# Optimization experiments

Hardware: AMD Instinct MI355X
Metric: run time of the kernel (lower is better)

## Reference

```python
import jax, jax.numpy as jnp
import numpy as np

EMBEDDING_DIM = 64  # matches init_kwargs; temperature = sqrt(embedding_dim)


def setup_inputs() -> dict:
    key = jax.random.key(0)
    k1, k2, k3, k4 = jax.random.split(key, 4)
    B, S, D = 8, 2048, EMBEDDING_DIM
    return {
        "key": jax.random.normal(k1, (B, S, D), dtype=jnp.float32),
        "query": jax.random.normal(k2, (B, S, D), dtype=jnp.float32),
        "value": jax.random.normal(k3, (B, S, D), dtype=jnp.float32),
        "query_attention_mask": jax.random.randint(k4, (B, S), 0, 2, dtype=jnp.int32),
    }


def reference(key, query, value, query_attention_mask):
    # scores: [B, S, S]
    temperature = jnp.sqrt(jnp.asarray(EMBEDDING_DIM, dtype=query.dtype))
    scores = jnp.einsum("bqd,bkd->bqk", query, key) / temperature
    # masked_fill_ fills -inf WHERE mask is True (as in the torch source).
    # mask [B, S] -> broadcast over the query axis to [B, 1, S] -> [B, S, S].
    mask = query_attention_mask.astype(bool)[:, None, :]
    scores = jnp.where(mask, -jnp.inf, scores)
    attention_filter = jax.nn.softmax(scores, axis=-1)
    # dropout p=0.0 (deterministic reference) -> identity
    context = jnp.einsum("bqk,bkd->bqd", attention_filter, value)
    return (context, attention_filter)
```

## Files before the change

kernel.cpp:

```cpp
#include <hip/hip_runtime.h>
#include <hip/hip_bf16.h>
#include <math.h>


typedef short bf16x8 __attribute__((ext_vector_type(8)));
typedef short bf16x4 __attribute__((ext_vector_type(4)));
typedef float f32x4 __attribute__((ext_vector_type(4)));

#define BATCH 8
#define SDIM 2048
#define DDIM 64
#define KBLK 64
#define NBLK (SDIM / KBLK)
#define SCALE 0.125f

__device__ __forceinline__ short f2bf(float f) {
    unsigned x = __float_as_uint(f);
    x = (x + 0x7fffu + ((x >> 16) & 1u)) >> 16;
    return (short)x;
}

__device__ __forceinline__ float fidx(const float4& v, int i) {
    return ((const float*)&v)[i];
}

__global__ __launch_bounds__(256, 1)
void attn_fused(const float* __restrict__ Kg, const float* __restrict__ Qg,
                const float* __restrict__ Vg, const int* __restrict__ Mg,
                float* __restrict__ Ctx, float* __restrict__ Filt)
{
    __shared__ short Klds[KBLK][72];
    __shared__ short VTlds[DDIM][72];
    __shared__ float Plds[4][16][68];
    __shared__ int   Mlds[KBLK];

    const int wg = blockIdx.x;
    const int b = wg & 7;
    const int qtile = wg >> 3;
    const int tid = threadIdx.x;
    const int w = tid >> 6;
    const int lane = tid & 63;
    const int col = lane & 15;
    const int quad = lane >> 4;

    const float* Kb = Kg + (size_t)b * SDIM * DDIM;
    const float* Qb = Qg + (size_t)b * SDIM * DDIM;
    const float* Vb = Vg + (size_t)b * SDIM * DDIM;
    const int*   Mb = Mg + (size_t)b * SDIM;
    float* Ctxb  = Ctx  + (size_t)b * SDIM * DDIM;
    float* Filtb = Filt + (size_t)b * SDIM * SDIM;

    const int qrow = qtile * 64 + w * 16 + col;

    bf16x8 aq[2];
    {
        const float* qsrc = Qb + (size_t)qrow * DDIM + quad * 8;
        #pragma unroll
        for (int c = 0; c < 2; ++c) {
            float4 f0 = *(const float4*)(qsrc + c * 32);
            float4 f1 = *(const float4*)(qsrc + c * 32 + 4);
            bf16x8 a;
            a[0]=f2bf(f0.x); a[1]=f2bf(f0.y); a[2]=f2bf(f0.z); a[3]=f2bf(f0.w);
            a[4]=f2bf(f1.x); a[5]=f2bf(f1.y); a[6]=f2bf(f1.z); a[7]=f2bf(f1.w);
            aq[c] = a;
        }
    }

    const int sk_key = tid >> 2;
    const int sk_d0  = (tid & 3) * 16;
    const int sv_d0  = (tid & 15) * 4;
    const int sv_k0  = (tid >> 4) * 4;

    float m_run[4], l_run[4];
    #pragma unroll
    for (int r = 0; r < 4; ++r) { m_run[r] = -1e30f; l_run[r] = 0.0f; }

    float4 kreg[4];
    int mreg = 0;
    {
        const float* src = Kb + (size_t)sk_key * DDIM + sk_d0;
        #pragma unroll
        for (int i = 0; i < 4; ++i) kreg[i] = *(const float4*)(src + i * 4);
        if (tid < KBLK) mreg = Mb[tid];
    }

    for (int kb = 0; kb < NBLK; ++kb) {
        __syncthreads();
        {
            bf16x8 p0, p1;
            p0[0]=f2bf(kreg[0].x); p0[1]=f2bf(kreg[0].y); p0[2]=f2bf(kreg[0].z); p0[3]=f2bf(kreg[0].w);
            p0[4]=f2bf(kreg[1].x); p0[5]=f2bf(kreg[1].y); p0[6]=f2bf(kreg[1].z); p0[7]=f2bf(kreg[1].w);
            p1[0]=f2bf(kreg[2].x); p1[1]=f2bf(kreg[2].y); p1[2]=f2bf(kreg[2].z); p1[3]=f2bf(kreg[2].w);
            p1[4]=f2bf(kreg[3].x); p1[5]=f2bf(kreg[3].y); p1[6]=f2bf(kreg[3].z); p1[7]=f2bf(kreg[3].w);
            *(bf16x8*)&Klds[sk_key][sk_d0]     = p0;
            *(bf16x8*)&Klds[sk_key][sk_d0 + 8] = p1;
            if (tid < KBLK) Mlds[tid] = mreg;
        }
        __syncthreads();
        if (kb + 1 < NBLK) {
            const float* src = Kb + (size_t)((kb + 1) * KBLK + sk_key) * DDIM + sk_d0;
            #pragma unroll
            for (int i = 0; i < 4; ++i) kreg[i] = *(const float4*)(src + i * 4);
            if (tid < KBLK) mreg = Mb[(kb + 1) * KBLK + tid];
        }

        float s[4][4];
        #pragma unroll
        for (int t = 0; t < 4; ++t) {
            f32x4 acc = {0.f, 0.f, 0.f, 0.f};
            #pragma unroll
            for (int c = 0; c < 2; ++c) {
                bf16x8 bk = *(const bf16x8*)&Klds[t * 16 + col][c * 32 + quad * 8];
                acc = __builtin_amdgcn_mfma_f32_16x16x32_bf16(aq[c], bk, acc, 0, 0, 0);
            }
            const int mk = Mlds[t * 16 + col];
            #pragma unroll
            for (int r = 0; r < 4; ++r)
                s[t][r] = mk ? -INFINITY : acc[r] * SCALE;
        }
        #pragma unroll
        for (int r = 0; r < 4; ++r) {
            float mx = fmaxf(fmaxf(s[0][r], s[1][r]), fmaxf(s[2][r], s[3][r]));
            mx = fmaxf(mx, __shfl_xor(mx, 1));
            mx = fmaxf(mx, __shfl_xor(mx, 2));
            mx = fmaxf(mx, __shfl_xor(mx, 4));
            mx = fmaxf(mx, __shfl_xor(mx, 8));
            const float mn = fmaxf(m_run[r], mx);
            float sum = __expf(s[0][r] - mn) + __expf(s[1][r] - mn)
                      + __expf(s[2][r] - mn) + __expf(s[3][r] - mn);
            sum += __shfl_xor(sum, 1);
            sum += __shfl_xor(sum, 2);
            sum += __shfl_xor(sum, 4);
            sum += __shfl_xor(sum, 8);
            l_run[r] = l_run[r] * __expf(m_run[r] - mn) + sum;
            m_run[r] = mn;
        }
    }

    float inv_l[4];
    #pragma unroll
    for (int r = 0; r < 4; ++r) inv_l[r] = 1.0f / l_run[r];

    f32x4 Oacc[4];
    #pragma unroll
    for (int dt = 0; dt < 4; ++dt) Oacc[dt] = (f32x4){0.f, 0.f, 0.f, 0.f};

    float4 vreg[4];
    {
        const float* srck = Kb + (size_t)sk_key * DDIM + sk_d0;
        #pragma unroll
        for (int i = 0; i < 4; ++i) kreg[i] = *(const float4*)(srck + i * 4);
        const float* srcv = Vb + (size_t)sv_k0 * DDIM + sv_d0;
        #pragma unroll
        for (int i = 0; i < 4; ++i) vreg[i] = *(const float4*)(srcv + (size_t)i * DDIM);
        if (tid < KBLK) mreg = Mb[tid];
    }

    for (int kb = 0; kb < NBLK; ++kb) {
        __syncthreads();
        {
            bf16x8 p0, p1;
            p0[0]=f2bf(kreg[0].x); p0[1]=f2bf(kreg[0].y); p0[2]=f2bf(kreg[0].z); p0[3]=f2bf(kreg[0].w);
            p0[4]=f2bf(kreg[1].x); p0[5]=f2bf(kreg[1].y); p0[6]=f2bf(kreg[1].z); p0[7]=f2bf(kreg[1].w);
            p1[0]=f2bf(kreg[2].x); p1[1]=f2bf(kreg[2].y); p1[2]=f2bf(kreg[2].z); p1[3]=f2bf(kreg[2].w);
            p1[4]=f2bf(kreg[3].x); p1[5]=f2bf(kreg[3].y); p1[6]=f2bf(kreg[3].z); p1[7]=f2bf(kreg[3].w);
            *(bf16x8*)&Klds[sk_key][sk_d0]     = p0;
            *(bf16x8*)&Klds[sk_key][sk_d0 + 8] = p1;
            #pragma unroll
            for (int dd = 0; dd < 4; ++dd) {
                bf16x4 pv;
                pv[0] = f2bf(fidx(vreg[0], dd));
                pv[1] = f2bf(fidx(vreg[1], dd));
                pv[2] = f2bf(fidx(vreg[2], dd));
                pv[3] = f2bf(fidx(vreg[3], dd));
                *(bf16x4*)&VTlds[sv_d0 + dd][sv_k0] = pv;
            }
            if (tid < KBLK) Mlds[tid] = mreg;
        }
        __syncthreads();
        if (kb + 1 < NBLK) {
            const float* srck = Kb + (size_t)((kb + 1) * KBLK + sk_key) * DDIM + sk_d0;
            #pragma unroll
            for (int i = 0; i < 4; ++i) kreg[i] = *(const float4*)(srck + i * 4);
            const float* srcv = Vb + (size_t)((kb + 1) * KBLK + sv_k0) * DDIM + sv_d0;
            #pragma unroll
            for (int i = 0; i < 4; ++i) vreg[i] = *(const float4*)(srcv + (size_t)i * DDIM);
            if (tid < KBLK) mreg = Mb[(kb + 1) * KBLK + tid];
        }

        #pragma unroll
        for (int t = 0; t < 4; ++t) {
            f32x4 acc = {0.f, 0.f, 0.f, 0.f};
            #pragma unroll
            for (int c = 0; c < 2; ++c) {
                bf16x8 bk = *(const bf16x8*)&Klds[t * 16 + col][c * 32 + quad * 8];
                acc = __builtin_amdgcn_mfma_f32_16x16x32_bf16(aq[c], bk, acc, 0, 0, 0);
            }
            const int mk = Mlds[t * 16 + col];
            #pragma unroll
            for (int r = 0; r < 4; ++r) {
                float p = mk ? 0.0f : __expf(acc[r] * SCALE - m_run[r]) * inv_l[r];
                Plds[w][quad * 4 + r][t * 16 + col] = p;
            }
        }

        #pragma unroll
        for (int i = 0; i < 4; ++i) {
            const int row = i * 4 + quad;
            float4 pv = *(const float4*)&Plds[w][row][col * 4];
            *(float4*)(Filtb + (size_t)(qtile * 64 + w * 16 + row) * SDIM + kb * KBLK + col * 4) = pv;
        }

        #pragma unroll
        for (int c = 0; c < 2; ++c) {
            float4 pa0 = *(const float4*)&Plds[w][col][c * 32 + quad * 8];
            float4 pa1 = *(const float4*)&Plds[w][col][c * 32 + quad * 8 + 4];
            bf16x8 ap;
            ap[0]=f2bf(pa0.x); ap[1]=f2bf(pa0.y); ap[2]=f2bf(pa0.z); ap[3]=f2bf(pa0.w);
            ap[4]=f2bf(pa1.x); ap[5]=f2bf(pa1.y); ap[6]=f2bf(pa1.z); ap[7]=f2bf(pa1.w);
            #pragma unroll
            for (int dt = 0; dt < 4; ++dt) {
                bf16x8 bv = *(const bf16x8*)&VTlds[dt * 16 + col][c * 32 + quad * 8];
                Oacc[dt] = __builtin_amdgcn_mfma_f32_16x16x32_bf16(ap, bv, Oacc[dt], 0, 0, 0);
            }
        }
    }

    #pragma unroll
    for (int dt = 0; dt < 4; ++dt) {
        #pragma unroll
        for (int r = 0; r < 4; ++r) {
            Ctxb[(size_t)(qtile * 64 + w * 16 + quad * 4 + r) * DDIM + dt * 16 + col] = Oacc[dt][r];
        }
    }
}

extern "C" void kernel_launch(void* const* d_in, const int* in_sizes, int n_in,
                              void* d_out, int out_size, void* d_ws, size_t ws_size,
                              hipStream_t stream) {
    const float* Kg = (const float*)d_in[0];
    const float* Qg = (const float*)d_in[1];
    const float* Vg = (const float*)d_in[2];
    const int*   Mg = (const int*)d_in[3];
    float* Ctx  = (float*)d_out;
    float* Filt = (float*)d_out + (size_t)BATCH * SDIM * DDIM;

    dim3 grid(BATCH * (SDIM / 64));
    dim3 block(256);
    attn_fused<<<grid, block, 0, stream>>>(Kg, Qg, Vg, Mg, Ctx, Filt);
}
```

Measured before the change: 214.5 us.

## Split key axis across workgroups with stats/merge/emit kernels and atomic context accumulation

Splits the fused attention kernel into three launches. A stats pass computes per-split row max and sum over a quarter of the keys, a merge pass combines them and zeroes the context, and an emit pass writes the probabilities and accumulates context with atomic adds. This gives four times more workgroups and higher occupancy, so the MI355X CUs fill better than with 256 workgroups. The P tile is now stored as bf16 in LDS and the probability matrix is written straight from registers instead of being staged through LDS. The costs are two extra launches, atomic contention on the context, and probability stores that are less coalesced.

New measurement: 202.7 us. -5.5%, faster.

```diff
diff --git a/kernel.cpp b/kernel.cpp
--- a/kernel.cpp
+++ b/kernel.cpp
@@ -12,49 +12,42 @@
 #define DDIM 64
 #define KBLK 64
 #define NBLK (SDIM / KBLK)
+#define KSPLIT 4
+#define BPW (NBLK / KSPLIT)
+#define NROWS (BATCH * SDIM)
 #define SCALE 0.125f
+#define KSTR 66
 
 __device__ __forceinline__ short f2bf(float f) {
     unsigned x = __float_as_uint(f);
     x = (x + 0x7fffu + ((x >> 16) & 1u)) >> 16;
     return (short)x;
 }
-
 __device__ __forceinline__ float fidx(const float4& v, int i) {
     return ((const float*)&v)[i];
 }
 
-__global__ __launch_bounds__(256, 1)
-void attn_fused(const float* __restrict__ Kg, const float* __restrict__ Qg,
-                const float* __restrict__ Vg, const int* __restrict__ Mg,
-                float* __restrict__ Ctx, float* __restrict__ Filt)
+__global__ __launch_bounds__(256, 4)
+void attn_stats(const float* __restrict__ Kg, const float* __restrict__ Qg,
+                const int* __restrict__ Mg, float2* __restrict__ part)
 {
-    __shared__ short Klds[KBLK][72];
-    __shared__ short VTlds[DDIM][72];
-    __shared__ float Plds[4][16][68];
+    __shared__ short Klds[KBLK][KSTR];
     __shared__ int   Mlds[KBLK];
 
     const int wg = blockIdx.x;
     const int b = wg & 7;
-    const int qtile = wg >> 3;
+    const int qt = (wg >> 3) & 31;
+    const int sp = wg >> 8;
     const int tid = threadIdx.x;
-    const int w = tid >> 6;
-    const int lane = tid & 63;
-    const int col = lane & 15;
-    const int quad = lane >> 4;
+    const int w = tid >> 6, lane = tid & 63, col = lane & 15, quad = lane >> 4;
 
     const float* Kb = Kg + (size_t)b * SDIM * DDIM;
     const float* Qb = Qg + (size_t)b * SDIM * DDIM;
-    const float* Vb = Vg + (size_t)b * SDIM * DDIM;
     const int*   Mb = Mg + (size_t)b * SDIM;
-    float* Ctxb  = Ctx  + (size_t)b * SDIM * DDIM;
-    float* Filtb = Filt + (size_t)b * SDIM * SDIM;
-
-    const int qrow = qtile * 64 + w * 16 + col;
 
     bf16x8 aq[2];
     {
-        const float* qsrc = Qb + (size_t)qrow * DDIM + quad * 8;
+        const float* qsrc = Qb + (size_t)(qt * 64 + w * 16 + col) * DDIM + quad * 8;
         #pragma unroll
         for (int c = 0; c < 2; ++c) {
             float4 f0 = *(const float4*)(qsrc + c * 32);
@@ -68,8 +61,7 @@
 
     const int sk_key = tid >> 2;
     const int sk_d0  = (tid & 3) * 16;
-    const int sv_d0  = (tid & 15) * 4;
-    const int sv_k0  = (tid >> 4) * 4;
+    const int kb0 = sp * BPW * KBLK;
 
     float m_run[4], l_run[4];
     #pragma unroll
@@ -78,13 +70,13 @@
     float4 kreg[4];
     int mreg = 0;
     {
-        const float* src = Kb + (size_t)sk_key * DDIM + sk_d0;
+        const float* src = Kb + (size_t)(kb0 + sk_key) * DDIM + sk_d0;
         #pragma unroll
         for (int i = 0; i < 4; ++i) kreg[i] = *(const float4*)(src + i * 4);
-        if (tid < KBLK) mreg = Mb[tid];
-    }
-
-    for (int kb = 0; kb < NBLK; ++kb) {
+        if (tid < KBLK) mreg = Mb[kb0 + tid];
+    }
+
+    for (int kb = 0; kb < BPW; ++kb) {
         __syncthreads();
         {
             bf16x8 p0, p1;
@@ -97,11 +89,11 @@
             if (tid < KBLK) Mlds[tid] = mreg;
         }
         __syncthreads();
-        if (kb + 1 < NBLK) {
-            const float* src = Kb + (size_t)((kb + 1) * KBLK + sk_key) * DDIM + sk_d0;
+        if (kb + 1 < BPW) {
+            const float* src = Kb + (size_t)(kb0 + (kb + 1) * KBLK + sk_key) * DDIM + sk_d0;
             #pragma unroll
             for (int i = 0; i < 4; ++i) kreg[i] = *(const float4*)(src + i * 4);
-            if (tid < KBLK) mreg = Mb[(kb + 1) * KBLK + tid];
+            if (tid < KBLK) mreg = Mb[kb0 + (kb + 1) * KBLK + tid];
         }
 
         float s[4][4];
@@ -137,26 +129,108 @@
         }
     }
 
-    float inv_l[4];
+    if (col == 0) {
+        #pragma unroll
+        for (int r = 0; r < 4; ++r)
+            part[(size_t)sp * NROWS + b * SDIM + qt * 64 + w * 16 + quad * 4 + r] =
+                make_float2(m_run[r], l_run[r]);
+    }
+}
+
+__global__ __launch_bounds__(256)
+void attn_merge(const float2* __restrict__ part, float2* __restrict__ stats,
+                float* __restrict__ Ctx)
+{
+    const int t = blockIdx.x * 256 + threadIdx.x;
+    if (t < NROWS) {
+        float mp[KSPLIT], lp[KSPLIT];
+        #pragma unroll
+        for (int sp = 0; sp < KSPLIT; ++sp) {
+            float2 v = part[(size_t)sp * NROWS + t];
+            mp[sp] = v.x; lp[sp] = v.y;
+        }
+        float m = fmaxf(fmaxf(mp[0], mp[1]), fmaxf(mp[2], mp[3]));
+        float l = 0.f;
+        #pragma unroll
+        for (int sp = 0; sp < KSPLIT; ++sp) l += lp[sp] * __expf(mp[sp] - m);
+        stats[t] = make_float2(m, 1.0f / l);
+    }
+    float4* C4 = (float4*)Ctx;
+    const int n4 = BATCH * SDIM * DDIM / 4;
+    const int nthr = gridDim.x * 256;
+    for (int i = t; i < n4; i += nthr) C4[i] = make_float4(0.f, 0.f, 0.f, 0.f);
+}
+
+__global__ __launch_bounds__(256, 4)
+void attn_emit(const float* __restrict__ Kg, const float* __restrict__ Vg,
+               const float* __restrict__ Qg, const int* __restrict__ Mg,
+               const float2* __restrict__ stats, float* __restrict__ Ctx,
+               float* __restrict__ Filt)
+{
+    __shared__ short Klds[KBLK][KSTR];
+    __shared__ short VTlds[DDIM][KSTR];
+    __shared__ short Plds[4][16][KSTR];
+    __shared__ int   Mlds[KBLK];
+
+    const int wg = blockIdx.x;
+    const int b = wg & 7;
+    const int qt = (wg >> 3) & 31;
+    const int sp = wg >> 8;
+    const int tid = threadIdx.x;
+    const int w = tid >> 6, lane = tid & 63, col = lane & 15, quad = lane >> 4;
+
+    const float* Kb = Kg + (size_t)b * SDIM * DDIM;
+    const float* Qb = Qg + (size_t)b * SDIM * DDIM;
+    const float* Vb = Vg + (size_t)b * SDIM * DDIM;
+    const int*   Mb = Mg + (size_t)b * SDIM;
+    float* Ctxb  = Ctx  + (size_t)b * SDIM * DDIM;
+    float* Filtb = Filt + (size_t)b * SDIM * SDIM;
+
+    bf16x8 aq[2];
+    {
+        const float* qsrc = Qb + (size_t)(qt * 64 + w * 16 + col) * DDIM + quad * 8;
+        #pragma unroll
+        for (int c = 0; c < 2; ++c) {
+            float4 f0 = *(const float4*)(qsrc + c * 32);
+            float4 f1 = *(const float4*)(qsrc + c * 32 + 4);
+            bf16x8 a;
+            a[0]=f2bf(f0.x); a[1]=f2bf(f0.y); a[2]=f2bf(f0.z); a[3]=f2bf(f0.w);
+            a[4]=f2bf(f1.x); a[5]=f2bf(f1.y); a[6]=f2bf(f1.z); a[7]=f2bf(f1.w);
+            aq[c] = a;
+        }
+    }
+
+    float mrow[4], invl[4];
     #pragma unroll
-    for (int r = 0; r < 4; ++r) inv_l[r] = 1.0f / l_run[r];
+    for (int r = 0; r < 4; ++r) {
+        float2 s2 = stats[b * SDIM + qt * 64 + w * 16 + quad * 4 + r];
+        mrow[r] = s2.x; invl[r] = s2.y;
+    }
+
+    const int sk_key = tid >> 2;
+    const int sk_d0  = (tid & 3) * 16;
+    const int sv_d0  = (tid & 15) * 4;
+    const int sv_k0  = (tid >> 4) * 4;
+    const int kb0 = sp * BPW * KBLK;
 
     f32x4 Oacc[4];
     #pragma unroll
     for (int dt = 0; dt < 4; ++dt) Oacc[dt] = (f32x4){0.f, 0.f, 0.f, 0.f};
 
-    float4 vreg[4];
+    float4 kreg[4], vreg[4];
+    int mreg = 0;
     {
-        const float* srck = Kb + (size_t)sk_key * DDIM + sk_d0;
+        const float* srck = Kb + (size_t)(kb0 + sk_key) * DDIM + sk_d0;
         #pragma unroll
         for (int i = 0; i < 4; ++i) kreg[i] = *(const float4*)(srck + i * 4);
-        const float* srcv = Vb + (size_t)sv_k0 * DDIM + sv_d0;
+        const float* srcv = Vb + (size_t)(kb0 + sv_k0) * DDIM + sv_d0;
         #pragma unroll
         for (int i = 0; i < 4; ++i) vreg[i] = *(const float4*)(srcv + (size_t)i * DDIM);
-        if (tid < KBLK) mreg = Mb[tid];
-    }
-
-    for (int kb = 0; kb < NBLK; ++kb) {
+        if (tid < KBLK) mreg = Mb[kb0 + tid];
+    }
+
+    for (int kb = 0; kb < BPW; ++kb) {
+        const int kbase = kb0 + kb * KBLK;
         __syncthreads();
         {
             bf16x8 p0, p1;
@@ -178,14 +252,14 @@
             if (tid < KBLK) Mlds[tid] = mreg;
         }
         __syncthreads();
-        if (kb + 1 < NBLK) {
-            const float* srck = Kb + (size_t)((kb + 1) * KBLK + sk_key) * DDIM + sk_d0;
+        if (kb + 1 < BPW) {
+            const float* srck = Kb + (size_t)(kb0 + (kb + 1) * KBLK + sk_key) * DDIM + sk_d0;
             #pragma unroll
             for (int i = 0; i < 4; ++i) kreg[i] = *(const float4*)(srck + i * 4);
-            const float* srcv = Vb + (size_t)((kb + 1) * KBLK + sv_k0) * DDIM + sv_d0;
+            const float* srcv = Vb + (size_t)(kb0 + (kb + 1) * KBLK + sv_k0) * DDIM + sv_d0;
             #pragma unroll
             for (int i = 0; i < 4; ++i) vreg[i] = *(const float4*)(srcv + (size_t)i * DDIM);
-            if (tid < KBLK) mreg = Mb[(kb + 1) * KBLK + tid];
+            if (tid < KBLK) mreg = Mb[kb0 + (kb + 1) * KBLK + tid];
         }
 
         #pragma unroll
@@ -199,25 +273,15 @@
             const int mk = Mlds[t * 16 + col];
             #pragma unroll
             for (int r = 0; r < 4; ++r) {
-                float p = mk ? 0.0f : __expf(acc[r] * SCALE - m_run[r]) * inv_l[r];
-                Plds[w][quad * 4 + r][t * 16 + col] = p;
-            }
-        }
-
-        #pragma unroll
-        for (int i = 0; i < 4; ++i) {
-            const int row = i * 4 + quad;
-            float4 pv = *(const float4*)&Plds[w][row][col * 4];
-            *(float4*)(Filtb + (size_t)(qtile * 64 + w * 16 + row) * SDIM + kb * KBLK + col * 4) = pv;
+                float p = mk ? 0.0f : __expf(acc[r] * SCALE - mrow[r]) * invl[r];
+                Filtb[(size_t)(qt * 64 + w * 16 + quad * 4 + r) * SDIM + kbase + t * 16 + col] = p;
+                Plds[w][quad * 4 + r][t * 16 + col] = f2bf(p);
+            }
         }
 
         #pragma unroll
         for (int c = 0; c < 2; ++c) {
-            float4 pa0 = *(const float4*)&Plds[w][col][c * 32 + quad * 8];
-            float4 pa1 = *(const float4*)&Plds[w][col][c * 32 + quad * 8 + 4];
-            bf16x8 ap;
-            ap[0]=f2bf(pa0.x); ap[1]=f2bf(pa0.y); ap[2]=f2bf(pa0.z); ap[3]=f2bf(pa0.w);
-            ap[4]=f2bf(pa1.x); ap[5]=f2bf(pa1.y); ap[6]=f2bf(pa1.z); ap[7]=f2bf(pa1.w);
+            bf16x8 ap = *(const bf16x8*)&Plds[w][col][c * 32 + quad * 8];
             #pragma unroll
             for (int dt = 0; dt < 4; ++dt) {
                 bf16x8 bv = *(const bf16x8*)&VTlds[dt * 16 + col][c * 32 + quad * 8];
@@ -230,7 +294,8 @@
     for (int dt = 0; dt < 4; ++dt) {
         #pragma unroll
         for (int r = 0; r < 4; ++r) {
-            Ctxb[(size_t)(qtile * 64 + w * 16 + quad * 4 + r) * DDIM + dt * 16 + col] = Oacc[dt][r];
+            unsafeAtomicAdd(&Ctxb[(size_t)(qt * 64 + w * 16 + quad * 4 + r) * DDIM + dt * 16 + col],
+                            Oacc[dt][r]);
         }
     }
 }
@@ -245,7 +310,10 @@
     float* Ctx  = (float*)d_out;
     float* Filt = (float*)d_out + (size_t)BATCH * SDIM * DDIM;
 
-    dim3 grid(BATCH * (SDIM / 64));
-    dim3 block(256);
-    attn_fused<<<grid, block, 0, stream>>>(Kg, Qg, Vg, Mg, Ctx, Filt);
-}
+    float2* part  = (float2*)d_ws;
+    float2* stats = part + (size_t)KSPLIT * NROWS;
+
+    attn_stats<<<dim3(BATCH * NBLK * KSPLIT), dim3(256), 0, stream>>>(Kg, Qg, Mg, part);
+    attn_merge<<<dim3(256), dim3(256), 0, stream>>>(part, stats, Ctx);
+    attn_emit<<<dim3(BATCH * NBLK * KSPLIT), dim3(256), 0, stream>>>(Kg, Vg, Qg, Mg, stats, Ctx, Filt);
+}
```
